# Kernel tuning notes

Hardware: AMD Instinct MI355X
Metric: run time of the kernel (lower is better)

Reference implementation:

```python
import jax, jax.numpy as jnp
import numpy as np

B, S, T = 4, 1024, 1024
CTX, QIN, C, H = 1024, 1024, 1024, 16
HD = C // H  # per-head channels


def setup_inputs() -> dict:
    key = jax.random.key(0)
    ks = jax.random.split(key, 12)
    s = 0.02
    return {
        "query": jax.random.normal(ks[0], (B, S, QIN), jnp.float32),
        "key": jax.random.normal(ks[1], (B, T, CTX), jnp.float32),
        "value": jax.random.normal(ks[2], (B, T, CTX), jnp.float32),
        "mask": jax.random.randint(ks[3], (B, S, T), 0, 2).astype(bool),
        "Wq": jax.random.normal(ks[4], (C, QIN), jnp.float32) * s,
        "bq": jax.random.normal(ks[5], (C,), jnp.float32) * s,
        "Wk": jax.random.normal(ks[6], (C, CTX), jnp.float32) * s,
        "bk": jax.random.normal(ks[7], (C,), jnp.float32) * s,
        "Wv": jax.random.normal(ks[8], (C, CTX), jnp.float32) * s,
        "bv": jax.random.normal(ks[9], (C,), jnp.float32) * s,
        "Wo": jax.random.normal(ks[10], (C, C), jnp.float32) * s,
        "bo": jax.random.normal(ks[11], (C,), jnp.float32) * s,
    }


def reference(query, key, value, mask, Wq, bq, Wk, bk, Wv, bv, Wo, bo):
    b, s, _ = query.shape
    t = key.shape[1]
    c = Wq.shape[0]
    h, hd = H, c // H
    q = (query @ Wq.T + bq).reshape(b, s, h, hd)
    k = (key @ Wk.T + bk).reshape(b, t, h, hd)
    v = (value @ Wv.T + bv).reshape(b, t, h, hd)
    # [B,H,S,T] scores, scaled by 1/sqrt(head_dim)
    score = jnp.einsum('bshd,bthd->bhst', q, k) * (hd ** -0.5)
    # masked_fill_(~mask[:, None, 0:1], -inf): mask key positions via row 0
    score = jnp.where(mask[:, None, 0:1], score, -jnp.inf)
    weights = jax.nn.softmax(score, axis=-1)
    out = jnp.einsum('bhst,bthd->bshd', weights, v).reshape(b, s, c)
    out = out @ Wo.T + bo
    out = out * mask[..., 0:1].astype(out.dtype)
    return out
```

## Files before the change

### kernel.cpp

```cpp
#include <hip/hip_runtime.h>
#include <stdint.h>

#define Bb  4
#define Ss  1024
#define Tt  1024
#define Cc  1024
#define Hh  16
#define HDd 64
#define Kk  1024

typedef __bf16 bf16;
typedef __bf16 bf16x8 __attribute__((ext_vector_type(8)));
typedef float  f32x4  __attribute__((ext_vector_type(4)));
typedef __attribute__((address_space(1))) uint32_t gu32;
typedef __attribute__((address_space(3))) uint32_t lu32;

__device__ __forceinline__ void load_lds16(const bf16* g, bf16* l) {
    __builtin_amdgcn_global_load_lds((gu32*)g, (lu32*)l, 16, 0, 0);
}

#define BARRIER_LDS() do {                                    \
    asm volatile("s_waitcnt lgkmcnt(0)" ::: "memory");        \
    __builtin_amdgcn_s_barrier();                             \
} while (0)

#define BARRIER_VM() do {                                     \
    asm volatile("s_waitcnt vmcnt(0)" ::: "memory");          \
    __builtin_amdgcn_s_barrier();                             \
} while (0)

__global__ void cvt8(const float* __restrict__ s0, const float* __restrict__ s1,
                     const float* __restrict__ s2, const float* __restrict__ s3,
                     const float* __restrict__ s4, const float* __restrict__ s5,
                     const float* __restrict__ s6,
                     bf16* __restrict__ d0, bf16* __restrict__ d1,
                     bf16* __restrict__ d2, bf16* __restrict__ d3,
                     bf16* __restrict__ d4, bf16* __restrict__ d5,
                     bf16* __restrict__ d6)
{
    const float* s; bf16* d; int n;
    switch (blockIdx.y) {
        case 0: s = s0; d = d0; n = Bb * Ss * Kk; break;
        case 1: s = s1; d = d1; n = Bb * Ss * Kk; break;
        case 2: s = s2; d = d2; n = Bb * Ss * Kk; break;
        case 3: s = s3; d = d3; n = Cc * Kk; break;
        case 4: s = s4; d = d4; n = Cc * Kk; break;
        case 5: s = s5; d = d5; n = Cc * Kk; break;
        default: s = s6; d = d6; n = Cc * Kk; break;
    }
    const int i = (blockIdx.x * blockDim.x + threadIdx.x) * 8;
    if (i >= n) return;
    const float4 a = *(const float4*)(s + i);
    const float4 c = *(const float4*)(s + i + 4);
    bf16x8 o;
    o[0] = (bf16)a.x; o[1] = (bf16)a.y; o[2] = (bf16)a.z; o[3] = (bf16)a.w;
    o[4] = (bf16)c.x; o[5] = (bf16)c.y; o[6] = (bf16)c.z; o[7] = (bf16)c.w;
    *(bf16x8*)(d + i) = o;
}

__device__ __forceinline__ void mainloop_128x64_pf(
    const bf16* __restrict__ Ab, const bf16* __restrict__ Wb,
    bf16* As, bf16* Bs, f32x4 acc[4][2])
{
    const int tid  = threadIdx.x;
    const int wid  = tid >> 6;
    const int lane = tid & 63;
    const int l16  = lane & 15;
    const int quad = lane >> 4;
    const int wm   = wid >> 1;
    const int wn   = wid & 1;
    const int r8   = lane >> 3;
    const int ssw  = ((lane & 7) ^ r8) * 8;

    auto stage = [&](int k0) {
#pragma unroll
        for (int p = 0; p < 4; p++) {
            const int rb = wid * 32 + p * 8;
            load_lds16(Ab + (size_t)(rb + r8) * Kk + k0 + ssw, As + rb * 64);
        }
#pragma unroll
        for (int p = 0; p < 2; p++) {
            const int rb = wid * 16 + p * 8;
            load_lds16(Wb + (size_t)(rb + r8) * Kk + k0 + ssw, Bs + rb * 64);
        }
    };

    stage(0);
    BARRIER_VM();

    for (int k0 = 0; k0 < Kk; k0 += 64) {
        bf16x8 af[2][4], bw[2][2];
#pragma unroll
        for (int kh = 0; kh < 2; kh++) {
#pragma unroll
            for (int i = 0; i < 4; i++)
                af[kh][i] = *(const bf16x8*)(As + (wm * 64 + i * 16 + l16) * 64 +
                                             (((kh * 4 + quad) ^ (l16 & 7)) * 8));
#pragma unroll
            for (int j = 0; j < 2; j++)
                bw[kh][j] = *(const bf16x8*)(Bs + (wn * 32 + j * 16 + l16) * 64 +
                                             (((kh * 4 + quad) ^ (l16 & 7)) * 8));
        }
        BARRIER_LDS();
        if (k0 + 64 < Kk) stage(k0 + 64);
#pragma unroll
        for (int kh = 0; kh < 2; kh++)
#pragma unroll
            for (int i = 0; i < 4; i++)
#pragma unroll
                for (int j = 0; j < 2; j++)
                    acc[i][j] = __builtin_amdgcn_mfma_f32_16x16x32_bf16(af[kh][i], bw[kh][j], acc[i][j], 0, 0, 0);
        BARRIER_VM();
    }
}

__global__ __launch_bounds__(256)
void gemm_qkv(const bf16* __restrict__ Aq, const bf16* __restrict__ Ak, const bf16* __restrict__ Av,
              const bf16* __restrict__ Wq, const bf16* __restrict__ Wk, const bf16* __restrict__ Wv,
              const float* __restrict__ bq, const float* __restrict__ bk, const float* __restrict__ bv,
              bf16* __restrict__ Oq, bf16* __restrict__ Ok, bf16* __restrict__ Ov)
{
    __shared__ __align__(16) bf16 As[128 * 64];
    __shared__ __align__(16) bf16 Bs[64 * 64];
    const int z = blockIdx.z;
    const bf16*  A    = (z == 0) ? Aq : (z == 1) ? Ak : Av;
    const bf16*  W    = (z == 0) ? Wq : (z == 1) ? Wk : Wv;
    const float* bias = (z == 0) ? bq : (z == 1) ? bk : bv;
    bf16*        O    = (z == 0) ? Oq : (z == 1) ? Ok : Ov;

    f32x4 acc[4][2];
    const f32x4 z4 = {0.f, 0.f, 0.f, 0.f};
#pragma unroll
    for (int i = 0; i < 4; i++)
#pragma unroll
        for (int j = 0; j < 2; j++) acc[i][j] = z4;

    mainloop_128x64_pf(A + (size_t)blockIdx.x * 128 * Kk,
                       W + (size_t)blockIdx.y * 64 * Kk, As, Bs, acc);

    const int tid = threadIdx.x;
    const int wid = tid >> 6, lane = tid & 63;
    const int l16 = lane & 15, quad = lane >> 4;
    const int wm = wid >> 1, wn = wid & 1;
    const int row0 = blockIdx.x * 128 + wm * 64;
    const int col0 = blockIdx.y * 64 + wn * 32;
#pragma unroll
    for (int j = 0; j < 2; j++) {
        const int col = col0 + j * 16 + l16;
        const float bj = bias[col];
        const int h = col >> 6, d = col & 63;
#pragma unroll
        for (int i = 0; i < 4; i++) {
#pragma unroll
            for (int r = 0; r < 4; r++) {
                const int row = row0 + i * 16 + quad * 4 + r;
                const int b = row >> 10, s = row & 1023;
                const bf16 val = (bf16)(acc[i][j][r] + bj);
                if (z == 2) {
                    Ov[((size_t)((b * Hh + h) * HDd + d)) * Tt + s] = val;
                } else {
                    O[((size_t)(b * Hh + h) * Ss + s) * HDd + d] = val;
                }
            }
        }
    }
}

__global__ __launch_bounds__(256)
void gemm_out(const bf16* __restrict__ A, const bf16* __restrict__ W,
              const float* __restrict__ bias, const int* __restrict__ mask,
              float* __restrict__ out)
{
    __shared__ __align__(16) bf16 As[128 * 64];
    __shared__ __align__(16) bf16 Bs[64 * 64];
    f32x4 acc[4][2];
    const f32x4 z4 = {0.f, 0.f, 0.f, 0.f};
#pragma unroll
    for (int i = 0; i < 4; i++)
#pragma unroll
        for (int j = 0; j < 2; j++) acc[i][j] = z4;

    mainloop_128x64_pf(A + (size_t)blockIdx.x * 128 * Kk,
                       W + (size_t)blockIdx.y * 64 * Kk, As, Bs, acc);

    const int tid = threadIdx.x;
    const int wid = tid >> 6, lane = tid & 63;
    const int l16 = lane & 15, quad = lane >> 4;
    const int wm = wid >> 1, wn = wid & 1;
    const int row0 = blockIdx.x * 128 + wm * 64;
    const int col0 = blockIdx.y * 64 + wn * 32;
#pragma unroll
    for (int j = 0; j < 2; j++) {
        const int col = col0 + j * 16 + l16;
        const float bj = bias[col];
#pragma unroll
        for (int i = 0; i < 4; i++) {
#pragma unroll
            for (int r = 0; r < 4; r++) {
                const int row = row0 + i * 16 + quad * 4 + r;
                const float mval = (mask[(size_t)row * Tt] != 0) ? 1.f : 0.f;
                out[(size_t)row * Cc + col] = (acc[i][j][r] + bj) * mval;
            }
        }
    }
}

__global__ __launch_bounds__(256, 2)
void attn(const bf16* __restrict__ Q, const bf16* __restrict__ Kp, const bf16* __restrict__ Vt,
          const int* __restrict__ mask, bf16* __restrict__ X)
{
    __shared__ __align__(16) bf16 Ks[64 * 64];
    __shared__ __align__(16) bf16 Vs[64 * 64];
    __shared__ __align__(16) bf16 Ps[4][32 * 72];
    const int g   = blockIdx.x;
    const int xcd = g & 7, idx = g >> 3;
    const int bh  = xcd * 8 + (idx >> 3);
    const int qblk = idx & 7;
    const int b = bh >> 4, h = bh & 15;
    const int tid = threadIdx.x, wid = tid >> 6, lane = tid & 63;
    const int l16 = lane & 15, quad = lane >> 4;
    const bf16* Qbh = Q  + (size_t)bh * Ss * HDd;
    const bf16* Kbh = Kp + (size_t)bh * Tt * HDd;
    const bf16* Vbh = Vt + (size_t)bh * HDd * Tt;
    const int*  mb  = mask + (size_t)b * Ss * Tt;
    const int q0 = qblk * 128 + wid * 32;
    bf16* Psw = &Ps[wid][0];

    bf16x8 qf[2][2];
#pragma unroll
    for (int u = 0; u < 2; u++) {
        qf[u][0] = *(const bf16x8*)(Qbh + (size_t)(q0 + u * 16 + l16) * HDd + quad * 8);
        qf[u][1] = *(const bf16x8*)(Qbh + (size_t)(q0 + u * 16 + l16) * HDd + 32 + quad * 8);
    }

    float ls[2][4];
    f32x4 o[2][4];
    const f32x4 z4 = {0.f, 0.f, 0.f, 0.f};
#pragma unroll
    for (int u = 0; u < 2; u++)
#pragma unroll
        for (int r = 0; r < 4; r++) ls[u][r] = 0.f;
#pragma unroll
    for (int u = 0; u < 2; u++)
#pragma unroll
        for (int dblk = 0; dblk < 4; dblk++) o[u][dblk] = z4;

    const int srow = lane >> 3;
    const int schk = lane & 7;
    const int sswz = (schk ^ srow) * 8;
    const int c80 = wid * 2, c81 = wid * 2 + 1;

    const bf16* kg0 = Kbh + (size_t)(c80 * 8 + srow) * HDd + sswz;
    const bf16* kg1 = Kbh + (size_t)(c81 * 8 + srow) * HDd + sswz;
    const bf16* vg0 = Vbh + (size_t)(c80 * 8 + srow) * Tt + sswz;
    const bf16* vg1 = Vbh + (size_t)(c81 * 8 + srow) * Tt + sswz;
    bf16* kd0 = Ks + c80 * 512 + lane * 8;
    bf16* kd1 = Ks + c81 * 512 + lane * 8;
    bf16* vd0 = Vs + c80 * 512 + lane * 8;
    bf16* vd1 = Vs + c81 * 512 + lane * 8;

    bf16x8 ka0, ka1, va0, va1;
    bf16x8 kb0, kb1, vb0, vb1;
    int mA0, mA1, mA2, mA3, mB0, mB1, mB2, mB3;

#define LOADA(KT) do { const int _kt = (KT);                          \
    ka0 = *(const bf16x8*)(kg0 + (size_t)_kt * HDd);                  \
    ka1 = *(const bf16x8*)(kg1 + (size_t)_kt * HDd);                  \
    va0 = *(const bf16x8*)(vg0 + _kt);                                \
    va1 = *(const bf16x8*)(vg1 + _kt);                                \
    mA0 = mb[_kt + l16];      mA1 = mb[_kt + 16 + l16];               \
    mA2 = mb[_kt + 32 + l16]; mA3 = mb[_kt + 48 + l16]; } while (0)
#define LOADB(KT) do { const int _kt = (KT);                          \
    kb0 = *(const bf16x8*)(kg0 + (size_t)_kt * HDd);                  \
    kb1 = *(const bf16x8*)(kg1 + (size_t)_kt * HDd);                  \
    vb0 = *(const bf16x8*)(vg0 + _kt);                                \
    vb1 = *(const bf16x8*)(vg1 + _kt);                                \
    mB0 = mb[_kt + l16];      mB1 = mb[_kt + 16 + l16];               \
    mB2 = mb[_kt + 32 + l16]; mB3 = mb[_kt + 48 + l16]; } while (0)
#define STOREA() do {                                                 \
    *(bf16x8*)kd0 = ka0; *(bf16x8*)kd1 = ka1;                         \
    *(bf16x8*)vd0 = va0; *(bf16x8*)vd1 = va1; } while (0)
#define STOREB() do {                                                 \
    *(bf16x8*)kd0 = kb0; *(bf16x8*)kd1 = kb1;                         \
    *(bf16x8*)vd0 = vb0; *(bf16x8*)vd1 = vb1; } while (0)

    auto compute = [&](int m0, int m1, int m2, int m3) {
        f32x4 sc[2][4];
#pragma unroll
        for (int u = 0; u < 2; u++)
#pragma unroll
            for (int nb = 0; nb < 4; nb++) sc[u][nb] = z4;
#pragma unroll
        for (int nb = 0; nb < 4; nb++) {
            const bf16* krow = Ks + (nb * 16 + l16) * 64;
            const bf16x8 kf0 = *(const bf16x8*)(krow + ((quad       ^ (l16 & 7)) * 8));
            const bf16x8 kf1 = *(const bf16x8*)(krow + (((4 + quad) ^ (l16 & 7)) * 8));
#pragma unroll
            for (int u = 0; u < 2; u++) {
                sc[u][nb] = __builtin_amdgcn_mfma_f32_16x16x32_bf16(qf[u][0], kf0, sc[u][nb], 0, 0, 0);
                sc[u][nb] = __builtin_amdgcn_mfma_f32_16x16x32_bf16(qf[u][1], kf1, sc[u][nb], 0, 0, 0);
            }
        }

        const int mm[4] = {m0, m1, m2, m3};
#pragma unroll
        for (int nb = 0; nb < 4; nb++) {
            const float madd = mm[nb] ? 0.f : -1e30f;
#pragma unroll
            for (int u = 0; u < 2; u++) {
#pragma unroll
                for (int r = 0; r < 4; r++) {
                    const float p = __expf(sc[u][nb][r] * 0.125f + madd);
                    ls[u][r] += p;
                    Psw[(u * 16 + quad * 4 + r) * 72 + nb * 16 + l16] = (bf16)p;
                }
            }
        }

#pragma unroll
        for (int kh = 0; kh < 2; kh++) {
            const bf16x8 pf0 = *(const bf16x8*)(Psw + (l16) * 72 + kh * 32 + quad * 8);
            const bf16x8 pf1 = *(const bf16x8*)(Psw + (16 + l16) * 72 + kh * 32 + quad * 8);
#pragma unroll
            for (int dblk = 0; dblk < 4; dblk++) {
                const bf16x8 vf = *(const bf16x8*)(Vs + (dblk * 16 + l16) * 64 +
                                                   (((kh * 4 + quad) ^ (l16 & 7)) * 8));
                o[0][dblk] = __builtin_amdgcn_mfma_f32_16x16x32_bf16(pf0, vf, o[0][dblk], 0, 0, 0);
                o[1][dblk] = __builtin_amdgcn_mfma_f32_16x16x32_bf16(pf1, vf, o[1][dblk], 0, 0, 0);
            }
        }
    };

    LOADA(0);

    for (int kt = 0; kt < Tt; kt += 128) {
        BARRIER_LDS();
        LOADB(kt + 64);
        STOREA();
        BARRIER_LDS();
        compute(mA0, mA1, mA2, mA3);

        BARRIER_LDS();
        LOADA((kt + 128 < Tt) ? (kt + 128) : (Tt - 64));
        STOREB();
        BARRIER_LDS();
        compute(mB0, mB1, mB2, mB3);
    }
#undef LOADA
#undef LOADB
#undef STOREA
#undef STOREB

#pragma unroll
    for (int off = 1; off <= 8; off <<= 1)
#pragma unroll
        for (int u = 0; u < 2; u++)
#pragma unroll
            for (int r = 0; r < 4; r++)
                ls[u][r] += __shfl_xor(ls[u][r], off, 64);
    float inv[2][4];
#pragma unroll
    for (int u = 0; u < 2; u++)
#pragma unroll
        for (int r = 0; r < 4; r++) inv[u][r] = 1.f / ls[u][r];

#pragma unroll
    for (int u = 0; u < 2; u++) {
#pragma unroll
        for (int dblk = 0; dblk < 4; dblk++) {
#pragma unroll
            for (int r = 0; r < 4; r++) {
                const int srow_q = q0 + u * 16 + quad * 4 + r;
                const int d = dblk * 16 + l16;
                X[(size_t)(b * Ss + srow_q) * Cc + h * HDd + d] = (bf16)(o[u][dblk][r] * inv[u][r]);
            }
        }
    }
}

extern "C" void kernel_launch(void* const* d_in, const int* in_sizes, int n_in,
                              void* d_out, int out_size, void* d_ws, size_t ws_size,
                              hipStream_t stream)
{
    const float* query = (const float*)d_in[0];
    const float* key   = (const float*)d_in[1];
    const float* value = (const float*)d_in[2];
    const int*   mask  = (const int*)d_in[3];
    const float* Wq = (const float*)d_in[4];
    const float* bq = (const float*)d_in[5];
    const float* Wk = (const float*)d_in[6];
    const float* bk = (const float*)d_in[7];
    const float* Wv = (const float*)d_in[8];
    const float* bv = (const float*)d_in[9];
    const float* Wo = (const float*)d_in[10];
    const float* bo = (const float*)d_in[11];
    float* out = (float*)d_out;

    char* ws = (char*)d_ws;
    const size_t MB = 1024 * 1024;
    bf16* qb  = (bf16*)(ws + 0 * MB);
    bf16* kb  = (bf16*)(ws + 8 * MB);
    bf16* vb  = (bf16*)(ws + 16 * MB);
    bf16* wqb = (bf16*)(ws + 24 * MB);
    bf16* wkb = (bf16*)(ws + 26 * MB);
    bf16* wvb = (bf16*)(ws + 28 * MB);
    bf16* wob = (bf16*)(ws + 30 * MB);
    bf16* Qp  = (bf16*)(ws + 32 * MB);
    bf16* Kpp = (bf16*)(ws + 40 * MB);
    bf16* Vtp = (bf16*)(ws + 48 * MB);
    bf16* Xb  = (bf16*)(ws + 56 * MB);

    cvt8<<<dim3(2048, 7), 256, 0, stream>>>(query, key, value, Wq, Wk, Wv, Wo,
                                            qb, kb, vb, wqb, wkb, wvb, wob);
    gemm_qkv<<<dim3(32, 16, 3), 256, 0, stream>>>(qb, kb, vb, wqb, wkb, wvb,
                                                  bq, bk, bv, Qp, Kpp, Vtp);
    attn<<<dim3(512), 256, 0, stream>>>(Qp, Kpp, Vtp, mask, Xb);
    gemm_out<<<dim3(32, 16), 256, 0, stream>>>(Xb, wob, bo, mask, out);
}
```

Baseline: 221.1 us.

## Compact unmasked keys/values in QKV epilogue and skip masked key tiles in attention

The K/V projection epilogue computes a prefix sum over mask row 0 and scatters only unmasked key/value rows into a compacted layout. Attention then counts the valid keys and iterates only up to the rounded-up count, replacing per-tile mask loads with an index bound check. This roughly halves the attention work for a random mask, but adds a serial per-block prefix scan, a memset of the V buffer, and a simpler non-prefetching GEMM mainloop for the QKV kernel.

```diff
diff --git a/kernel.cpp b/kernel.cpp
--- a/kernel.cpp
+++ b/kernel.cpp
@@ -58,7 +58,7 @@
     *(bf16x8*)(d + i) = o;
 }
 
-__device__ __forceinline__ void mainloop_128x64_pf(
+__device__ __forceinline__ void mainloop_128x64_nv(
     const bf16* __restrict__ Ab, const bf16* __restrict__ Wb,
     bf16* As, bf16* Bs, f32x4 acc[4][2])
 {
@@ -72,6 +72,53 @@
     const int r8   = lane >> 3;
     const int ssw  = ((lane & 7) ^ r8) * 8;
 
+    for (int k0 = 0; k0 < Kk; k0 += 64) {
+#pragma unroll
+        for (int p = 0; p < 4; p++) {
+            const int rb = wid * 32 + p * 8;
+            load_lds16(Ab + (size_t)(rb + r8) * Kk + k0 + ssw, As + rb * 64);
+        }
+#pragma unroll
+        for (int p = 0; p < 2; p++) {
+            const int rb = wid * 16 + p * 8;
+            load_lds16(Wb + (size_t)(rb + r8) * Kk + k0 + ssw, Bs + rb * 64);
+        }
+        __syncthreads();
+#pragma unroll
+        for (int kh = 0; kh < 2; kh++) {
+            bf16x8 af[4], bw[2];
+#pragma unroll
+            for (int i = 0; i < 4; i++)
+                af[i] = *(const bf16x8*)(As + (wm * 64 + i * 16 + l16) * 64 +
+                                         (((kh * 4 + quad) ^ (l16 & 7)) * 8));
+#pragma unroll
+            for (int j = 0; j < 2; j++)
+                bw[j] = *(const bf16x8*)(Bs + (wn * 32 + j * 16 + l16) * 64 +
+                                         (((kh * 4 + quad) ^ (l16 & 7)) * 8));
+#pragma unroll
+            for (int i = 0; i < 4; i++)
+#pragma unroll
+                for (int j = 0; j < 2; j++)
+                    acc[i][j] = __builtin_amdgcn_mfma_f32_16x16x32_bf16(af[i], bw[j], acc[i][j], 0, 0, 0);
+        }
+        __syncthreads();
+    }
+}
+
+__device__ __forceinline__ void mainloop_128x64_pf(
+    const bf16* __restrict__ Ab, const bf16* __restrict__ Wb,
+    bf16* As, bf16* Bs, f32x4 acc[4][2])
+{
+    const int tid  = threadIdx.x;
+    const int wid  = tid >> 6;
+    const int lane = tid & 63;
+    const int l16  = lane & 15;
+    const int quad = lane >> 4;
+    const int wm   = wid >> 1;
+    const int wn   = wid & 1;
+    const int r8   = lane >> 3;
+    const int ssw  = ((lane & 7) ^ r8) * 8;
+
     auto stage = [&](int k0) {
 #pragma unroll
         for (int p = 0; p < 4; p++) {
@@ -118,15 +165,17 @@
 void gemm_qkv(const bf16* __restrict__ Aq, const bf16* __restrict__ Ak, const bf16* __restrict__ Av,
               const bf16* __restrict__ Wq, const bf16* __restrict__ Wk, const bf16* __restrict__ Wv,
               const float* __restrict__ bq, const float* __restrict__ bk, const float* __restrict__ bv,
+              const int* __restrict__ mask,
               bf16* __restrict__ Oq, bf16* __restrict__ Ok, bf16* __restrict__ Ov)
 {
     __shared__ __align__(16) bf16 As[128 * 64];
     __shared__ __align__(16) bf16 Bs[64 * 64];
+    __shared__ int red[256];
+    __shared__ int jj[128];
     const int z = blockIdx.z;
     const bf16*  A    = (z == 0) ? Aq : (z == 1) ? Ak : Av;
     const bf16*  W    = (z == 0) ? Wq : (z == 1) ? Wk : Wv;
     const float* bias = (z == 0) ? bq : (z == 1) ? bk : bv;
-    bf16*        O    = (z == 0) ? Oq : (z == 1) ? Ok : Ov;
 
     f32x4 acc[4][2];
     const f32x4 z4 = {0.f, 0.f, 0.f, 0.f};
@@ -135,7 +184,7 @@
 #pragma unroll
         for (int j = 0; j < 2; j++) acc[i][j] = z4;
 
-    mainloop_128x64_pf(A + (size_t)blockIdx.x * 128 * Kk,
+    mainloop_128x64_nv(A + (size_t)blockIdx.x * 128 * Kk,
                        W + (size_t)blockIdx.y * 64 * Kk, As, Bs, acc);
 
     const int tid = threadIdx.x;
@@ -144,6 +193,29 @@
     const int wm = wid >> 1, wn = wid & 1;
     const int row0 = blockIdx.x * 128 + wm * 64;
     const int col0 = blockIdx.y * 64 + wn * 32;
+    const int bb = (blockIdx.x * 128) >> 10;
+    const int t0 = (blockIdx.x * 128) & 1023;
+
+    if (z != 0) {
+        const int* mrow = mask + (size_t)bb * Ss * Tt;
+        int psum = 0;
+        for (int t = tid; t < t0; t += 256) psum += (mrow[t] != 0);
+        red[tid] = psum;
+        __syncthreads();
+        for (int off = 128; off > 0; off >>= 1) {
+            if (tid < off) red[tid] += red[tid + off];
+            __syncthreads();
+        }
+        const int base = red[0];
+        if (tid < 128) jj[tid] = (mrow[t0 + tid] != 0);
+        __syncthreads();
+        if (tid == 0) {
+            int a = base;
+            for (int i = 0; i < 128; i++) { const int v = jj[i]; jj[i] = v ? a : -1; a += v; }
+        }
+        __syncthreads();
+    }
+
 #pragma unroll
     for (int j = 0; j < 2; j++) {
         const int col = col0 + j * 16 + l16;
@@ -153,13 +225,18 @@
         for (int i = 0; i < 4; i++) {
 #pragma unroll
             for (int r = 0; r < 4; r++) {
-                const int row = row0 + i * 16 + quad * 4 + r;
-                const int b = row >> 10, s = row & 1023;
+                const int local = wm * 64 + i * 16 + quad * 4 + r;
+                const int row = blockIdx.x * 128 + local;
                 const bf16 val = (bf16)(acc[i][j][r] + bj);
-                if (z == 2) {
-                    Ov[((size_t)((b * Hh + h) * HDd + d)) * Tt + s] = val;
+                if (z == 0) {
+                    const int s = row & 1023;
+                    Oq[((size_t)(bb * Hh + h) * Ss + s) * HDd + d] = val;
                 } else {
-                    O[((size_t)(b * Hh + h) * Ss + s) * HDd + d] = val;
+                    const int jc = jj[local];
+                    if (jc >= 0) {
+                        if (z == 2) Ov[((size_t)((bb * Hh + h) * HDd + d)) * Tt + jc] = val;
+                        else        Ok[((size_t)(bb * Hh + h) * Tt + jc) * HDd + d] = val;
+                    }
                 }
             }
         }
@@ -212,6 +289,7 @@
     __shared__ __align__(16) bf16 Ks[64 * 64];
     __shared__ __align__(16) bf16 Vs[64 * 64];
     __shared__ __align__(16) bf16 Ps[4][32 * 72];
+    __shared__ int red[256];
     const int g   = blockIdx.x;
     const int xcd = g & 7, idx = g >> 3;
     const int bh  = xcd * 8 + (idx >> 3);
@@ -226,6 +304,17 @@
     const int q0 = qblk * 128 + wid * 32;
     bf16* Psw = &Ps[wid][0];
 
+    int ps = 0;
+    for (int t = tid; t < Tt; t += 256) ps += (mb[t] != 0);
+    red[tid] = ps;
+    __syncthreads();
+    for (int off = 128; off > 0; off >>= 1) {
+        if (tid < off) red[tid] += red[tid + off];
+        __syncthreads();
+    }
+    const int nkb = red[0];
+    const int lim = ((nkb + 127) >> 7) << 7;
+
     bf16x8 qf[2][2];
 #pragma unroll
     for (int u = 0; u < 2; u++) {
@@ -261,22 +350,17 @@
 
     bf16x8 ka0, ka1, va0, va1;
     bf16x8 kb0, kb1, vb0, vb1;
-    int mA0, mA1, mA2, mA3, mB0, mB1, mB2, mB3;
 
 #define LOADA(KT) do { const int _kt = (KT);                          \
     ka0 = *(const bf16x8*)(kg0 + (size_t)_kt * HDd);                  \
     ka1 = *(const bf16x8*)(kg1 + (size_t)_kt * HDd);                  \
     va0 = *(const bf16x8*)(vg0 + _kt);                                \
-    va1 = *(const bf16x8*)(vg1 + _kt);                                \
-    mA0 = mb[_kt + l16];      mA1 = mb[_kt + 16 + l16];               \
-    mA2 = mb[_kt + 32 + l16]; mA3 = mb[_kt + 48 + l16]; } while (0)
+    va1 = *(const bf16x8*)(vg1 + _kt); } while (0)
 #define LOADB(KT) do { const int _kt = (KT);                          \
     kb0 = *(const bf16x8*)(kg0 + (size_t)_kt * HDd);                  \
     kb1 = *(const bf16x8*)(kg1 + (size_t)_kt * HDd);                  \
     vb0 = *(const bf16x8*)(vg0 + _kt);                                \
-    vb1 = *(const bf16x8*)(vg1 + _kt);                                \
-    mB0 = mb[_kt + l16];      mB1 = mb[_kt + 16 + l16];               \
-    mB2 = mb[_kt + 32 + l16]; mB3 = mb[_kt + 48 + l16]; } while (0)
+    vb1 = *(const bf16x8*)(vg1 + _kt); } while (0)
 #define STOREA() do {                                                 \
     *(bf16x8*)kd0 = ka0; *(bf16x8*)kd1 = ka1;                         \
     *(bf16x8*)vd0 = va0; *(bf16x8*)vd1 = va1; } while (0)
@@ -284,7 +368,7 @@
     *(bf16x8*)kd0 = kb0; *(bf16x8*)kd1 = kb1;                         \
     *(bf16x8*)vd0 = vb0; *(bf16x8*)vd1 = vb1; } while (0)
 
-    auto compute = [&](int m0, int m1, int m2, int m3) {
+    auto compute = [&](int base) {
         f32x4 sc[2][4];
 #pragma unroll
         for (int u = 0; u < 2; u++)
@@ -302,15 +386,14 @@
             }
         }
 
-        const int mm[4] = {m0, m1, m2, m3};
 #pragma unroll
         for (int nb = 0; nb < 4; nb++) {
-            const float madd = mm[nb] ? 0.f : -1e30f;
+            const bool vv = (base + nb * 16 + l16) < nkb;
 #pragma unroll
             for (int u = 0; u < 2; u++) {
 #pragma unroll
                 for (int r = 0; r < 4; r++) {
-                    const float p = __expf(sc[u][nb][r] * 0.125f + madd);
+                    const float p = vv ? __expf(sc[u][nb][r] * 0.125f) : 0.f;
                     ls[u][r] += p;
                     Psw[(u * 16 + quad * 4 + r) * 72 + nb * 16 + l16] = (bf16)p;
                 }
@@ -333,18 +416,18 @@
 
     LOADA(0);
 
-    for (int kt = 0; kt < Tt; kt += 128) {
+    for (int kt = 0; kt < lim; kt += 128) {
         BARRIER_LDS();
         LOADB(kt + 64);
         STOREA();
         BARRIER_LDS();
-        compute(mA0, mA1, mA2, mA3);
+        compute(kt);
 
         BARRIER_LDS();
-        LOADA((kt + 128 < Tt) ? (kt + 128) : (Tt - 64));
+        LOADA((kt + 128 < lim) ? (kt + 128) : (lim - 64));
         STOREB();
         BARRIER_LDS();
-        compute(mB0, mB1, mB2, mB3);
+        compute(kt + 64);
     }
 #undef LOADA
 #undef LOADB
@@ -410,10 +493,12 @@
     bf16* Vtp = (bf16*)(ws + 48 * MB);
     bf16* Xb  = (bf16*)(ws + 56 * MB);
 
+    hipMemsetAsync(Vtp, 0, 8 * MB, stream);
+
     cvt8<<<dim3(2048, 7), 256, 0, stream>>>(query, key, value, Wq, Wk, Wv, Wo,
                                             qb, kb, vb, wqb, wkb, wvb, wob);
     gemm_qkv<<<dim3(32, 16, 3), 256, 0, stream>>>(qb, kb, vb, wqb, wkb, wvb,
-                                                  bq, bk, bv, Qp, Kpp, Vtp);
+                                                  bq, bk, bv, mask, Qp, Kpp, Vtp);
     attn<<<dim3(512), 256, 0, stream>>>(Qp, Kpp, Vtp, mask, Xb);
     gemm_out<<<dim3(32, 16), 256, 0, stream>>>(Xb, wob, bo, mask, out);
 }
```

Result: no change. 218.0 us (-1.4%).
